# Performance work log

Hardware: AMD Instinct MI355X
Metric: run time of the kernel (lower is better)

The kernel has to match this reference:

```python
import jax, jax.numpy as jnp
from jax import lax
import numpy as np

B = 32768
H = 7
W = 7
EMB = 64
NUM_ACTIONS = 7
HIDDEN = 128
CNN_OUT = 64 * 3 * 3  # 576, from 7x7 input through the conv/pool stack


def setup_inputs() -> dict:
    key = jax.random.key(0)
    ks = jax.random.split(key, 20)
    frame = jax.random.randint(ks[0], (2, B, H, W, 3), 0, 11, dtype=jnp.int32)
    carried_col = jax.random.randint(ks[1], (2, B, 1), 0, 6, dtype=jnp.int32)
    carried_obj = jax.random.randint(ks[2], (2, B, 1), 0, 11, dtype=jnp.int32)

    def w(k, shape):
        return (jax.random.normal(k, shape, jnp.float32) * 0.05)

    return {
        "frame": frame,
        "carried_col": carried_col,
        "carried_obj": carried_obj,
        "conv1_w": w(ks[3], (16, 3, 2, 2)),  "conv1_b": jnp.zeros((16,), jnp.float32),
        "conv2_w": w(ks[4], (32, 16, 2, 2)), "conv2_b": jnp.zeros((32,), jnp.float32),
        "conv3_w": w(ks[5], (64, 32, 2, 2)), "conv3_b": jnp.zeros((64,), jnp.float32),
        "proj_w": w(ks[6], (EMB, CNN_OUT + 2)), "proj_b": jnp.zeros((EMB,), jnp.float32),
        "h1_w": w(ks[7], (HIDDEN, EMB * 2 + 4)), "h1_b": jnp.zeros((HIDDEN,), jnp.float32),
        "ln_g": jnp.ones((HIDDEN,), jnp.float32), "ln_b": jnp.zeros((HIDDEN,), jnp.float32),
        "h2_w": w(ks[8], (HIDDEN, HIDDEN)), "h2_b": jnp.zeros((HIDDEN,), jnp.float32),
        "h3_w": w(ks[9], (NUM_ACTIONS, HIDDEN)), "h3_b": jnp.zeros((NUM_ACTIONS,), jnp.float32),
    }


def _conv(x, wgt, b):
    # Conv2d(kernel=2, padding=1), NCHW
    y = lax.conv_general_dilated(x, wgt, (1, 1), [(1, 1), (1, 1)],
                                 dimension_numbers=("NCHW", "OIHW", "NCHW"))
    return y + b[None, :, None, None]


def _maxpool2(x):
    # MaxPool2d(2): window 2, stride 2, floor (VALID)
    return lax.reduce_window(x, -jnp.inf, lax.max, (1, 1, 2, 2), (1, 1, 2, 2), "VALID")


def _encode(fr, cc, co, p):
    x = fr.transpose(0, 3, 1, 2).astype(jnp.float32)  # [B,3,H,W]
    x = _maxpool2(jax.nn.relu(_conv(x, p["conv1_w"], p["conv1_b"])))  # [B,16,4,4]
    x = _maxpool2(jax.nn.relu(_conv(x, p["conv2_w"], p["conv2_b"])))  # [B,32,2,2]
    x = jax.nn.relu(_conv(x, p["conv3_w"], p["conv3_b"]))             # [B,64,3,3]
    feats = x.reshape(x.shape[0], -1)                                  # [B,576]
    carried = jnp.concatenate([cc, co], axis=-1).astype(jnp.float32)   # [B,2]
    comb = jnp.concatenate([feats, carried], axis=1)                   # [B,578]
    return jax.nn.relu(comb @ p["proj_w"].T + p["proj_b"])            # [B,64]


def _dir_pos(fr):
    # vectorized first-match of frame[...,0]==10 in row-major order
    b = fr.shape[0]
    mask = (fr[..., 0] == 10).reshape(b, -1)             # [B, H*W]
    has = jnp.any(mask, axis=-1)                         # [B]
    idx = jnp.argmax(mask, axis=-1)                      # first True (row-major)
    y = idx // W
    x = idx % W
    ch2 = fr[..., 2].reshape(b, -1)
    d_raw = jnp.take_along_axis(ch2, idx[:, None], axis=1)[:, 0] % 4
    d = jnp.where(has, d_raw, 0)                         # [B] int
    pos = jnp.stack([y.astype(jnp.float32) / (H - 1),
                     x.astype(jnp.float32) / (W - 1)], axis=-1)
    pos = jnp.where(has[:, None], pos, jnp.float32(0.5))  # [B,2]
    return d, pos


def _forward(frame, carried_col, carried_obj, p):
    curr_f, next_f = frame[0], frame[1]
    curr_emb = _encode(curr_f, carried_col[0], carried_obj[0], p)
    next_emb = _encode(next_f, carried_col[1], carried_obj[1], p)
    cd, cpos = _dir_pos(curr_f)
    nd, npos = _dir_pos(next_f)
    delta = ((nd - cd + 4) % 4).astype(jnp.float32)
    angle = delta * (2.0 * 3.14159 / 4.0)  # matches source constant
    dir_delta = jnp.stack([jnp.sin(angle), jnp.cos(angle)], axis=-1)  # [B,2]
    pos_delta = npos - cpos                                           # [B,2]
    comb = jnp.concatenate([curr_emb, next_emb, dir_delta, pos_delta], axis=-1)  # [B,132]
    h = comb @ p["h1_w"].T + p["h1_b"]
    mu = h.mean(-1, keepdims=True)
    var = ((h - mu) ** 2).mean(-1, keepdims=True)
    h = (h - mu) * lax.rsqrt(var + 1e-5) * p["ln_g"] + p["ln_b"]
    h = jax.nn.relu(h)  # dropout = identity in eval
    h = jax.nn.relu(h @ p["h2_w"].T + p["h2_b"])
    return h @ p["h3_w"].T + p["h3_b"]  # [B, num_actions]


def reference(frame, carried_col, carried_obj,
              conv1_w, conv1_b, conv2_w, conv2_b, conv3_w, conv3_b,
              proj_w, proj_b, h1_w, h1_b, ln_g, ln_b,
              h2_w, h2_b, h3_w, h3_b):
    p = dict(conv1_w=conv1_w, conv1_b=conv1_b, conv2_w=conv2_w, conv2_b=conv2_b,
             conv3_w=conv3_w, conv3_b=conv3_b, proj_w=proj_w, proj_b=proj_b,
             h1_w=h1_w, h1_b=h1_b, ln_g=ln_g, ln_b=ln_b,
             h2_w=h2_w, h2_b=h2_b, h3_w=h3_w, h3_b=h3_b)
    return _forward(frame, carried_col, carried_obj, p)
```

## Files before the change

### kernel.cpp

```cpp
#include <hip/hip_runtime.h>
#include <hip/hip_bf16.h>

#define BATCH 32768
#define NELEM 65536

typedef unsigned short u16;
typedef unsigned int u32;
typedef __attribute__((ext_vector_type(8))) short bf16x8;
typedef __attribute__((ext_vector_type(4))) float f32x4;

__device__ __forceinline__ float bf2f(u16 u) {
    union { u32 u; float f; } c; c.u = ((u32)u) << 16; return c.f;
}
__device__ __forceinline__ u16 f2bf(float f) {
    union { float f; u32 u; } c; c.f = f;
    u32 x = c.u;
    u32 r = (x + 0x7fffu + ((x >> 16) & 1u)) >> 16;
    return (u16)r;
}

__global__ __launch_bounds__(256) void k0_prep(const float* __restrict__ pw,
        const float* __restrict__ w2, const float* __restrict__ w3,
        const float* __restrict__ h2w, const float* __restrict__ h1w,
        const float* __restrict__ w1,
        u16* __restrict__ pwT, u16* __restrict__ w2r, u16* __restrict__ w3r,
        u16* __restrict__ h2hi, u16* __restrict__ h2lo,
        u16* __restrict__ h1hi, u16* __restrict__ h1lo,
        u16* __restrict__ w1hi, u16* __restrict__ w1lo) {
    int idx = blockIdx.x * 256 + threadIdx.x;
    if (idx < 38912) {
        int j = idx / 608, kk = idx - j * 608;
        float v = 0.f;
        if (kk < 576) {
            int p = kk >> 6, oc = kk & 63;
            v = pw[j * 578 + oc * 9 + p];
        } else if (kk < 578) {
            v = pw[j * 578 + kk];
        }
        pwT[idx] = f2bf(v);
    } else if (idx < 40960) {
        int i = idx - 38912;
        int oc = i >> 6, rem = i & 63, tap = rem >> 4, ic = rem & 15;
        w2r[i] = f2bf(w2[oc * 64 + ic * 4 + tap]);
    } else if (idx < 49152) {
        int i = idx - 40960;
        int oc = i >> 7, rem = i & 127, tap = rem >> 5, ic = rem & 31;
        w3r[i] = f2bf(w3[oc * 128 + ic * 4 + tap]);
    } else if (idx < 65536) {
        int i = idx - 49152;
        float v = h2w[i];
        u16 hi = f2bf(v);
        h2hi[i] = hi;
        h2lo[i] = f2bf(v - bf2f(hi));
    } else if (idx < 86016) {
        int i = idx - 65536;
        int j = i / 160, k = i - j * 160;
        float v = (k < 132) ? h1w[j * 132 + k] : 0.f;
        u16 hi = f2bf(v);
        h1hi[i] = hi;
        h1lo[i] = f2bf(v - bf2f(hi));
    } else if (idx < 86528) {
        int i = idx - 86016;
        int oc = i >> 5, k = i & 31;
        int ky = k >> 4, kx = (k >> 3) & 1, c = k & 7;
        float v = (c < 3) ? w1[oc * 12 + c * 4 + ky * 2 + kx] : 0.f;
        u16 hi = f2bf(v);
        w1hi[i] = hi;
        w1lo[i] = f2bf(v - bf2f(hi));
    }
}

__global__ __launch_bounds__(256) void kconv_all(const int* __restrict__ frame,
        const u16* __restrict__ w1hi, const u16* __restrict__ w1lo,
        const float* __restrict__ b1,
        const u16* __restrict__ w2r, const float* __restrict__ b2,
        const u16* __restrict__ w3r, const float* __restrict__ b3,
        const int* __restrict__ ccol, const int* __restrict__ cobj,
        const u16* __restrict__ pwT, const float* __restrict__ pb,
        float* __restrict__ comb, float4* __restrict__ fdir) {
    __shared__ u16 lds[24576];
    u16* p2L   = lds;
    u16* p1L   = lds + 4096;
    u16* frL   = lds + 12288;
    u16* featL = lds + 4096;
    int t = threadIdx.x;
    int l = t & 63;
    int wv = t >> 6;
    int col = l & 15;
    int kg = l >> 4;
    int e0 = blockIdx.x * 32;

    #pragma unroll
    for (int i = 0; i < 6; ++i) {
        int o = i * 256 + t;
        if (o < 1312) *(uint4*)(frL + o * 8) = make_uint4(0u, 0u, 0u, 0u);
    }

    {
        bf16x8 c1hi = *(const bf16x8*)(w1hi + col * 32 + kg * 8);
        bf16x8 c1lo = *(const bf16x8*)(w1lo + col * 32 + kg * 8);
        float c1b = b1[col];
        int ky1 = kg >> 1, kx1 = kg & 1;
        bool wr1 = (kg < 2);
        for (int h = 0; h < 2; ++h) {
            __syncthreads();
            const int* fbase = frame + (size_t)(e0 + h * 16) * 147;
            #pragma unroll
            for (int i = 0; i < 10; ++i) {
                int idx = i * 256 + t;
                if (idx < 2352) {
                    int le = idx / 147, r = idx - le * 147;
                    int cell = r / 3, c = r - cell * 3;
                    int y = cell / 7, x = cell - y * 7;
                    frL[le * 656 + (y + 1) * 72 + (x + 1) * 8 + c] = f2bf((float)fbase[idx]);
                }
            }
            __syncthreads();
            #pragma unroll
            for (int q = 0; q < 4; ++q) {
                int le = wv * 4 + q;
                const u16* eb = frL + le * 656;
                u16* op = p1L + (h * 16 + le) * 256;
                #pragma unroll
                for (int mt = 0; mt < 4; ++mt) {
                    int posA = mt * 16 + col;
                    int oy = posA >> 3, ox = posA & 7;
                    bf16x8 a = *(const bf16x8*)(eb + (oy + ky1) * 72 + (ox + kx1) * 8);
                    f32x4 acc = {0.f, 0.f, 0.f, 0.f};
                    acc = __builtin_amdgcn_mfma_f32_16x16x32_bf16(a, c1hi, acc, 0, 0, 0);
                    acc = __builtin_amdgcn_mfma_f32_16x16x32_bf16(a, c1lo, acc, 0, 0, 0);
                    float x0 = fmaxf(acc[0] + c1b, 0.f);
                    float x1 = fmaxf(acc[1] + c1b, 0.f);
                    float x2 = fmaxf(acc[2] + c1b, 0.f);
                    float x3 = fmaxf(acc[3] + c1b, 0.f);
                    float y0 = fmaxf(x0, x1);
                    float y1 = fmaxf(x2, x3);
                    float m0 = fmaxf(y0, __shfl_xor(y0, 32, 64));
                    float m1 = fmaxf(y1, __shfl_xor(y1, 32, 64));
                    if (wr1) {
                        op[(mt * 4 + kg * 2 + 0) * 16 + col] = f2bf(m0);
                        op[(mt * 4 + kg * 2 + 1) * 16 + col] = f2bf(m1);
                    }
                }
            }
            {
                int le = wv * 4 + kg;
                const u16* eb = frL + le * 656;
                int best = 49;
                #pragma unroll
                for (int q2 = 0; q2 < 4; ++q2) {
                    int cell = col + q2 * 16;
                    if (cell < 49) {
                        int y = cell / 7, x = cell - y * 7;
                        u16 v = eb[(y + 1) * 72 + (x + 1) * 8];
                        if (v == (u16)0x4120 && cell < best) best = cell;
                    }
                }
                best = min(best, __shfl_xor(best, 1, 64));
                best = min(best, __shfl_xor(best, 2, 64));
                best = min(best, __shfl_xor(best, 4, 64));
                best = min(best, __shfl_xor(best, 8, 64));
                if (col == 0) {
                    float dd = 0.f, py = 0.5f, px = 0.5f;
                    if (best < 49) {
                        int y = best / 7, x = best - y * 7;
                        u16 c2 = eb[(y + 1) * 72 + (x + 1) * 8 + 2];
                        dd = (float)(((int)bf2f(c2)) & 3);
                        py = (float)y / 6.0f;
                        px = (float)x / 6.0f;
                    }
                    fdir[e0 + h * 16 + le] = make_float4(dd, py, px, 0.f);
                }
            }
        }
    }
    __syncthreads();

    {
        bf16x8 bfrag[2][2];
        #pragma unroll
        for (int s = 0; s < 2; ++s)
            #pragma unroll
            for (int nt = 0; nt < 2; ++nt)
                bfrag[s][nt] = *(const bf16x8*)(w2r + (nt * 16 + col) * 64 + s * 32 + kg * 8);
        float bias2[2] = { b2[col], b2[16 + col] };
        int oy = col >> 2, ox = col & 3;
        int aoff[2]; bool aok[2];
        #pragma unroll
        for (int s = 0; s < 2; ++s) {
            int tap = 2 * s + (kg >> 1);
            int ky = tap >> 1, kx = tap & 1;
            int iy = oy - 1 + ky, ix = ox - 1 + kx;
            aok[s] = (iy >= 0 && ix >= 0);
            aoff[s] = (iy * 4 + ix) * 16 + (kg & 1) * 8;
        }
        #pragma unroll
        for (int q = 0; q < 8; ++q) {
            int e = wv * 8 + q;
            const u16* pbase = p1L + e * 256;
            bf16x8 a0 = {0,0,0,0,0,0,0,0}, a1 = {0,0,0,0,0,0,0,0};
            if (aok[0]) a0 = *(const bf16x8*)(pbase + aoff[0]);
            if (aok[1]) a1 = *(const bf16x8*)(pbase + aoff[1]);
            f32x4 acc0 = {0.f,0.f,0.f,0.f}, acc1 = {0.f,0.f,0.f,0.f};
            acc0 = __builtin_amdgcn_mfma_f32_16x16x32_bf16(a0, bfrag[0][0], acc0, 0, 0, 0);
            acc1 = __builtin_amdgcn_mfma_f32_16x16x32_bf16(a0, bfrag[0][1], acc1, 0, 0, 0);
            acc0 = __builtin_amdgcn_mfma_f32_16x16x32_bf16(a1, bfrag[1][0], acc0, 0, 0, 0);
            acc1 = __builtin_amdgcn_mfma_f32_16x16x32_bf16(a1, bfrag[1][1], acc1, 0, 0, 0);
            #pragma unroll
            for (int nt = 0; nt < 2; ++nt) {
                f32x4 acc = nt ? acc1 : acc0;
                float b = bias2[nt];
                float m0 = fmaxf(fmaxf(acc[0] + b, 0.f), fmaxf(acc[1] + b, 0.f));
                float m1 = fmaxf(fmaxf(acc[2] + b, 0.f), fmaxf(acc[3] + b, 0.f));
                float p0 = fmaxf(m0, __shfl_xor(m0, 16, 64));
                float p1 = fmaxf(m1, __shfl_xor(m1, 16, 64));
                if ((kg & 1) == 0) {
                    int qq = (kg >> 1) * 2;
                    u16* op = p2L + e * 128 + nt * 16 + col;
                    op[qq * 32]       = f2bf(p0);
                    op[(qq + 1) * 32] = f2bf(p1);
                }
            }
        }
    }
    __syncthreads();

    int colhi = col >> 3, collo = col & 7;
    {
        bf16x8 bfrag[4][4];
        #pragma unroll
        for (int s = 0; s < 4; ++s)
            #pragma unroll
            for (int nt = 0; nt < 4; ++nt)
                bfrag[s][nt] = *(const bf16x8*)(w3r + (nt * 16 + col) * 128 + s * 32 + kg * 8);
        float bias[4];
        #pragma unroll
        for (int nt = 0; nt < 4; ++nt) bias[nt] = b3[nt * 16 + col];

        auto do_tile = [&](int i) {
            int m0 = i * 16;
            int m = m0 + col;
            u32 elem = (u32)(((unsigned long long)(u32)m * 954437177ull) >> 33);
            int p = m - (int)elem * 9;
            int oy = (p * 86) >> 8;
            int ox = p - 3 * oy;
            const u16* pbase = p2L + elem * 128 + kg * 8;
            f32x4 acc[4];
            #pragma unroll
            for (int nt = 0; nt < 4; ++nt) {
                acc[nt][0] = 0.f; acc[nt][1] = 0.f; acc[nt][2] = 0.f; acc[nt][3] = 0.f;
            }
            #pragma unroll
            for (int s = 0; s < 4; ++s) {
                int ky = s >> 1, kx = s & 1;
                int iy = oy - 1 + ky, ix = ox - 1 + kx;
                bf16x8 a = {0,0,0,0,0,0,0,0};
                if (iy >= 0 && iy <= 1 && ix >= 0 && ix <= 1)
                    a = *(const bf16x8*)(pbase + (iy * 2 + ix) * 32);
                #pragma unroll
                for (int nt = 0; nt < 4; ++nt)
                    acc[nt] = __builtin_amdgcn_mfma_f32_16x16x32_bf16(a, bfrag[s][nt], acc[nt], 0, 0, 0);
            }
            #pragma unroll
            for (int r = 0; r < 4; ++r) {
                int mr = m0 + kg * 4 + r;
                u32 er = (u32)(((unsigned long long)(u32)mr * 954437177ull) >> 33);
                int pr = mr - (int)er * 9;
                int e7 = (int)(er & 7u);
                u16* fb = featL + er * 640 + collo;
                #pragma unroll
                for (int nt = 0; nt < 4; ++nt) {
                    int blk = (pr * 8 + nt * 2 + colhi) ^ e7;
                    fb[blk * 8] = f2bf(fmaxf(acc[nt][r] + bias[nt], 0.f));
                }
            }
        };
        #pragma unroll
        for (int u = 0; u < 4; ++u) do_tile(wv + u * 4);
        if (wv < 2) do_tile(16 + wv);
    }
    if (t < 32) {
        union { u16 s[8]; uint4 q; } b;
        b.s[0] = f2bf((float)ccol[e0 + t]);
        b.s[1] = f2bf((float)cobj[e0 + t]);
        #pragma unroll
        for (int i = 2; i < 8; ++i) b.s[i] = 0;
        *(uint4*)(featL + t * 640 + (72 ^ (t & 7)) * 8) = b.q;
    }
    __syncthreads();

    int rh = wv & 1, nh = wv >> 1;
    int m0g = e0 + rh * 16;
    const u16* arowb = featL + (rh * 16 + col) * 640;
    int rx = col & 7;
    const u16* brow = pwT + (nh * 32 + col) * 608 + kg * 8;
    f32x4 acc0 = {0.f,0.f,0.f,0.f}, acc1 = {0.f,0.f,0.f,0.f};
    #pragma unroll
    for (int k0 = 0; k0 < 608; k0 += 32) {
        bf16x8 a;
        if (k0 + kg * 8 < 584) {
            int L = (k0 >> 3) + kg;
            a = *(const bf16x8*)(arowb + (L ^ rx) * 8);
        } else {
            #pragma unroll
            for (int j = 0; j < 8; ++j) a[j] = 0;
        }
        bf16x8 b0 = *(const bf16x8*)(brow + k0);
        bf16x8 b1 = *(const bf16x8*)(brow + 16 * 608 + k0);
        acc0 = __builtin_amdgcn_mfma_f32_16x16x32_bf16(a, b0, acc0, 0, 0, 0);
        acc1 = __builtin_amdgcn_mfma_f32_16x16x32_bf16(a, b1, acc1, 0, 0, 0);
    }
    float* outbase = (m0g < BATCH) ? (comb + (size_t)m0g * 128)
                                   : (comb + (size_t)(m0g - BATCH) * 128 + 64);
    #pragma unroll
    for (int nt = 0; nt < 2; ++nt) {
        int n = nh * 32 + nt * 16 + col;
        float pbv = pb[n];
        f32x4 acc = nt ? acc1 : acc0;
        #pragma unroll
        for (int r = 0; r < 4; ++r) {
            outbase[(kg * 4 + r) * 128 + n] = fmaxf(acc[r] + pbv, 0.f);
        }
    }
}

__device__ __forceinline__ void split8(const float* __restrict__ x,
                                       bf16x8& hi, bf16x8& lo) {
    #pragma unroll
    for (int j = 0; j < 8; ++j) {
        u16 h = f2bf(x[j]);
        hi[j] = (short)h;
        lo[j] = (short)f2bf(x[j] - bf2f(h));
    }
}

__global__ __launch_bounds__(256) void kmlp(const float* __restrict__ comb,
        const float4* __restrict__ fdir,
        const u16* __restrict__ h1hi, const u16* __restrict__ h1lo,
        const float* __restrict__ h1b,
        const float* __restrict__ lng, const float* __restrict__ lnb,
        const u16* __restrict__ h2hi, const u16* __restrict__ h2lo,
        const float* __restrict__ h2b,
        const float* __restrict__ h3w, const float* __restrict__ h3b,
        float* __restrict__ out) {
    __shared__ float hL[64 * 132];
    int t = threadIdx.x;
    int l = t & 63;
    int col = l & 15;
    int kg = l >> 4;
    int wv = t >> 6;
    int mb = blockIdx.x * 64;

    {
        int gb = mb + wv * 16 + col;
        const float* arow = comb + (size_t)gb * 128 + kg * 8;
        const u16* bh = h1hi + col * 160 + kg * 8;
        const u16* bl = h1lo + col * 160 + kg * 8;
        f32x4 acc[8];
        #pragma unroll
        for (int nt = 0; nt < 8; ++nt) {
            acc[nt][0] = 0.f; acc[nt][1] = 0.f; acc[nt][2] = 0.f; acc[nt][3] = 0.f;
        }
        #pragma unroll
        for (int s = 0; s < 5; ++s) {
            float x[8];
            if (s < 4) {
                #pragma unroll
                for (int j = 0; j < 8; ++j) x[j] = arow[s * 32 + j];
            } else {
                #pragma unroll
                for (int j = 0; j < 8; ++j) x[j] = 0.f;
                if (kg == 0) {
                    float4 f0 = fdir[gb];
                    float4 f1 = fdir[gb + BATCH];
                    int delta = (((int)f1.x) - ((int)f0.x) + 4) & 3;
                    const float ANG = (float)(2.0 * 3.14159 / 4.0);
                    float angle = (float)delta * ANG;
                    x[0] = sinf(angle);
                    x[1] = cosf(angle);
                    x[2] = f1.y - f0.y;
                    x[3] = f1.z - f0.z;
                }
            }
            bf16x8 ahi, alo;
            split8(x, ahi, alo);
            #pragma unroll
            for (int nt = 0; nt < 8; ++nt) {
                bf16x8 bhiF = *(const bf16x8*)(bh + nt * 2560 + s * 32);
                bf16x8 bloF = *(const bf16x8*)(bl + nt * 2560 + s * 32);
                acc[nt] = __builtin_amdgcn_mfma_f32_16x16x32_bf16(ahi, bhiF, acc[nt], 0, 0, 0);
                acc[nt] = __builtin_amdgcn_mfma_f32_16x16x32_bf16(alo, bhiF, acc[nt], 0, 0, 0);
                acc[nt] = __builtin_amdgcn_mfma_f32_16x16x32_bf16(ahi, bloF, acc[nt], 0, 0, 0);
            }
        }
        #pragma unroll
        for (int nt = 0; nt < 8; ++nt) {
            float bv = h1b[nt * 16 + col];
            #pragma unroll
            for (int r = 0; r < 4; ++r)
                hL[(wv * 16 + kg * 4 + r) * 132 + nt * 16 + col] = acc[nt][r] + bv;
        }
    }
    __syncthreads();

    for (int rr = 0; rr < 16; ++rr) {
        float* rp = hL + (wv * 16 + rr) * 132 + l * 2;
        float2 v = *(const float2*)rp;
        float s = v.x + v.y;
        s += __shfl_xor(s, 1, 64);
        s += __shfl_xor(s, 2, 64);
        s += __shfl_xor(s, 4, 64);
        s += __shfl_xor(s, 8, 64);
        s += __shfl_xor(s, 16, 64);
        s += __shfl_xor(s, 32, 64);
        float mu = s * (1.0f / 128.0f);
        float d0 = v.x - mu, d1 = v.y - mu;
        float vs = d0 * d0 + d1 * d1;
        vs += __shfl_xor(vs, 1, 64);
        vs += __shfl_xor(vs, 2, 64);
        vs += __shfl_xor(vs, 4, 64);
        vs += __shfl_xor(vs, 8, 64);
        vs += __shfl_xor(vs, 16, 64);
        vs += __shfl_xor(vs, 32, 64);
        float rs = rsqrtf(vs * (1.0f / 128.0f) + 1e-5f);
        float2 o;
        o.x = fmaxf(d0 * rs * lng[l * 2]     + lnb[l * 2],     0.f);
        o.y = fmaxf(d1 * rs * lng[l * 2 + 1] + lnb[l * 2 + 1], 0.f);
        *(float2*)rp = o;
    }
    __syncthreads();

    {
        const float* arow = hL + (wv * 16 + col) * 132 + kg * 8;
        const u16* bh = h2hi + col * 128 + kg * 8;
        const u16* bl = h2lo + col * 128 + kg * 8;
        f32x4 acc[8];
        #pragma unroll
        for (int nt = 0; nt < 8; ++nt) {
            acc[nt][0] = 0.f; acc[nt][1] = 0.f; acc[nt][2] = 0.f; acc[nt][3] = 0.f;
        }
        #pragma unroll
        for (int s = 0; s < 4; ++s) {
            float x[8];
            #pragma unroll
            for (int j = 0; j < 8; ++j) x[j] = arow[s * 32 + j];
            bf16x8 ahi, alo;
            split8(x, ahi, alo);
            #pragma unroll
            for (int nt = 0; nt < 8; ++nt) {
                bf16x8 bhiF = *(const bf16x8*)(bh + nt * 2048 + s * 32);
                bf16x8 bloF = *(const bf16x8*)(bl + nt * 2048 + s * 32);
                acc[nt] = __builtin_amdgcn_mfma_f32_16x16x32_bf16(ahi, bhiF, acc[nt], 0, 0, 0);
                acc[nt] = __builtin_amdgcn_mfma_f32_16x16x32_bf16(alo, bhiF, acc[nt], 0, 0, 0);
                acc[nt] = __builtin_amdgcn_mfma_f32_16x16x32_bf16(ahi, bloF, acc[nt], 0, 0, 0);
            }
        }
        __syncthreads();
        #pragma unroll
        for (int nt = 0; nt < 8; ++nt) {
            float bv = h2b[nt * 16 + col];
            #pragma unroll
            for (int r = 0; r < 4; ++r)
                hL[(wv * 16 + kg * 4 + r) * 132 + nt * 16 + col] = fmaxf(acc[nt][r] + bv, 0.f);
        }
    }
    __syncthreads();

    {
        int row = t >> 2, jq = t & 3, j0 = jq * 2;
        const float* rp = hL + row * 132;
        float a0 = h3b[j0];
        float a1 = (jq < 3) ? h3b[j0 + 1] : 0.f;
        #pragma unroll 4
        for (int c = 0; c < 32; ++c) {
            float4 v = *(const float4*)(rp + c * 4);
            const float* wr0 = h3w + j0 * 128 + c * 4;
            a0 += v.x * wr0[0];
            a0 += v.y * wr0[1];
            a0 += v.z * wr0[2];
            a0 += v.w * wr0[3];
            if (jq < 3) {
                const float* wr1 = h3w + (j0 + 1) * 128 + c * 4;
                a1 += v.x * wr1[0];
                a1 += v.y * wr1[1];
                a1 += v.z * wr1[2];
                a1 += v.w * wr1[3];
            }
        }
        float* ob = out + (size_t)(mb + row) * 7;
        ob[j0] = a0;
        if (jq < 3) ob[j0 + 1] = a1;
    }
}

extern "C" void kernel_launch(void* const* d_in, const int* in_sizes, int n_in,
                              void* d_out, int out_size, void* d_ws, size_t ws_size,
                              hipStream_t stream) {
    const int*   frame = (const int*)d_in[0];
    const int*   ccol  = (const int*)d_in[1];
    const int*   cobj  = (const int*)d_in[2];
    const float* w1    = (const float*)d_in[3];
    const float* b1    = (const float*)d_in[4];
    const float* w2    = (const float*)d_in[5];
    const float* b2    = (const float*)d_in[6];
    const float* w3    = (const float*)d_in[7];
    const float* b3    = (const float*)d_in[8];
    const float* pw    = (const float*)d_in[9];
    const float* pb    = (const float*)d_in[10];
    const float* h1w   = (const float*)d_in[11];
    const float* h1b   = (const float*)d_in[12];
    const float* lng   = (const float*)d_in[13];
    const float* lnb   = (const float*)d_in[14];
    const float* h2w   = (const float*)d_in[15];
    const float* h2b   = (const float*)d_in[16];
    const float* h3w   = (const float*)d_in[17];
    const float* h3b   = (const float*)d_in[18];
    float* out = (float*)d_out;

    char* ws = (char*)d_ws;
    float* comb     = (float*)(ws + 0);
    float4* fdir    = (float4*)(ws + 33554432);
    u16*   pwT      = (u16*)(ws + 132120576);
    u16*   w2r      = (u16*)(ws + 132120576 + 131072);
    u16*   w3r      = (u16*)(ws + 132120576 + 139264);
    u16*   h2hi     = (u16*)(ws + 132120576 + 163840);
    u16*   h2lo     = (u16*)(ws + 132120576 + 196608);
    u16*   h1hi     = (u16*)(ws + 132120576 + 229376);
    u16*   h1lo     = (u16*)(ws + 132120576 + 270336);
    u16*   w1hi     = (u16*)(ws + 132120576 + 311296);
    u16*   w1lo     = (u16*)(ws + 132120576 + 312320);

    k0_prep<<<340, 256, 0, stream>>>(pw, w2, w3, h2w, h1w, w1,
                                     pwT, w2r, w3r, h2hi, h2lo, h1hi, h1lo,
                                     w1hi, w1lo);
    kconv_all<<<2048, 256, 0, stream>>>(frame, w1hi, w1lo, b1, w2r, b2,
                                        w3r, b3, ccol, cobj, pwT, pb, comb, fdir);
    kmlp<<<512, 256, 0, stream>>>(comb, fdir, h1hi, h1lo, h1b, lng, lnb,
                                  h2hi, h2lo, h2b, h3w, h3b, out);
}
```

Baseline: 231.0 us.

## Fuse conv encoder and MLP head into a single kernel via LDS handoff

Merges the conv/projection kernel and the MLP kernel into one. Each block now processes 16 batch items for both frames, so the current and next embeddings for a row sit in the same block. The comb and fdir intermediates stay in shared memory instead of going through global workspace, which removes a 16MB write and read plus one launch. In exchange the MLP stage works on only 16 rows per block, so each weight fetch is reused less and there are more barriers per block.

```diff
diff --git a/kernel.cpp b/kernel.cpp
--- a/kernel.cpp
+++ b/kernel.cpp
@@ -70,25 +70,44 @@
     }
 }
 
-__global__ __launch_bounds__(256) void kconv_all(const int* __restrict__ frame,
+__device__ __forceinline__ void split8(const float* __restrict__ x,
+                                       bf16x8& hi, bf16x8& lo) {
+    #pragma unroll
+    for (int j = 0; j < 8; ++j) {
+        u16 h = f2bf(x[j]);
+        hi[j] = (short)h;
+        lo[j] = (short)f2bf(x[j] - bf2f(h));
+    }
+}
+
+__global__ __launch_bounds__(256) void kall(const int* __restrict__ frame,
         const u16* __restrict__ w1hi, const u16* __restrict__ w1lo,
         const float* __restrict__ b1,
         const u16* __restrict__ w2r, const float* __restrict__ b2,
         const u16* __restrict__ w3r, const float* __restrict__ b3,
         const int* __restrict__ ccol, const int* __restrict__ cobj,
         const u16* __restrict__ pwT, const float* __restrict__ pb,
-        float* __restrict__ comb, float4* __restrict__ fdir) {
+        const u16* __restrict__ h1hi, const u16* __restrict__ h1lo,
+        const float* __restrict__ h1b,
+        const float* __restrict__ lng, const float* __restrict__ lnb,
+        const u16* __restrict__ h2hi, const u16* __restrict__ h2lo,
+        const float* __restrict__ h2b,
+        const float* __restrict__ h3w, const float* __restrict__ h3b,
+        float* __restrict__ out) {
     __shared__ u16 lds[24576];
+    __shared__ float4 fdirL[32];
     u16* p2L   = lds;
     u16* p1L   = lds + 4096;
     u16* frL   = lds + 12288;
     u16* featL = lds + 4096;
+    float* combL = (float*)lds;
+    float* hL    = (float*)(lds + 4096);
     int t = threadIdx.x;
     int l = t & 63;
     int wv = t >> 6;
     int col = l & 15;
     int kg = l >> 4;
-    int e0 = blockIdx.x * 32;
+    int b0 = blockIdx.x * 16;
 
     #pragma unroll
     for (int i = 0; i < 6; ++i) {
@@ -104,7 +123,7 @@
         bool wr1 = (kg < 2);
         for (int h = 0; h < 2; ++h) {
             __syncthreads();
-            const int* fbase = frame + (size_t)(e0 + h * 16) * 147;
+            const int* fbase = frame + ((size_t)b0 + (size_t)h * BATCH) * 147;
             #pragma unroll
             for (int i = 0; i < 10; ++i) {
                 int idx = i * 256 + t;
@@ -169,7 +188,7 @@
                         py = (float)y / 6.0f;
                         px = (float)x / 6.0f;
                     }
-                    fdir[e0 + h * 16 + le] = make_float4(dd, py, px, 0.f);
+                    fdirL[h * 16 + le] = make_float4(dd, py, px, 0.f);
                 }
             }
         }
@@ -280,87 +299,56 @@
         if (wv < 2) do_tile(16 + wv);
     }
     if (t < 32) {
+        int g = b0 + (t >> 4) * BATCH + (t & 15);
         union { u16 s[8]; uint4 q; } b;
-        b.s[0] = f2bf((float)ccol[e0 + t]);
-        b.s[1] = f2bf((float)cobj[e0 + t]);
+        b.s[0] = f2bf((float)ccol[g]);
+        b.s[1] = f2bf((float)cobj[g]);
         #pragma unroll
         for (int i = 2; i < 8; ++i) b.s[i] = 0;
         *(uint4*)(featL + t * 640 + (72 ^ (t & 7)) * 8) = b.q;
     }
     __syncthreads();
 
-    int rh = wv & 1, nh = wv >> 1;
-    int m0g = e0 + rh * 16;
-    const u16* arowb = featL + (rh * 16 + col) * 640;
-    int rx = col & 7;
-    const u16* brow = pwT + (nh * 32 + col) * 608 + kg * 8;
-    f32x4 acc0 = {0.f,0.f,0.f,0.f}, acc1 = {0.f,0.f,0.f,0.f};
-    #pragma unroll
-    for (int k0 = 0; k0 < 608; k0 += 32) {
-        bf16x8 a;
-        if (k0 + kg * 8 < 584) {
-            int L = (k0 >> 3) + kg;
-            a = *(const bf16x8*)(arowb + (L ^ rx) * 8);
-        } else {
-            #pragma unroll
-            for (int j = 0; j < 8; ++j) a[j] = 0;
-        }
-        bf16x8 b0 = *(const bf16x8*)(brow + k0);
-        bf16x8 b1 = *(const bf16x8*)(brow + 16 * 608 + k0);
-        acc0 = __builtin_amdgcn_mfma_f32_16x16x32_bf16(a, b0, acc0, 0, 0, 0);
-        acc1 = __builtin_amdgcn_mfma_f32_16x16x32_bf16(a, b1, acc1, 0, 0, 0);
-    }
-    float* outbase = (m0g < BATCH) ? (comb + (size_t)m0g * 128)
-                                   : (comb + (size_t)(m0g - BATCH) * 128 + 64);
-    #pragma unroll
-    for (int nt = 0; nt < 2; ++nt) {
-        int n = nh * 32 + nt * 16 + col;
-        float pbv = pb[n];
-        f32x4 acc = nt ? acc1 : acc0;
-        #pragma unroll
-        for (int r = 0; r < 4; ++r) {
-            outbase[(kg * 4 + r) * 128 + n] = fmaxf(acc[r] + pbv, 0.f);
-        }
-    }
-}
-
-__device__ __forceinline__ void split8(const float* __restrict__ x,
-                                       bf16x8& hi, bf16x8& lo) {
-    #pragma unroll
-    for (int j = 0; j < 8; ++j) {
-        u16 h = f2bf(x[j]);
-        hi[j] = (short)h;
-        lo[j] = (short)f2bf(x[j] - bf2f(h));
-    }
-}
-
-__global__ __launch_bounds__(256) void kmlp(const float* __restrict__ comb,
-        const float4* __restrict__ fdir,
-        const u16* __restrict__ h1hi, const u16* __restrict__ h1lo,
-        const float* __restrict__ h1b,
-        const float* __restrict__ lng, const float* __restrict__ lnb,
-        const u16* __restrict__ h2hi, const u16* __restrict__ h2lo,
-        const float* __restrict__ h2b,
-        const float* __restrict__ h3w, const float* __restrict__ h3b,
-        float* __restrict__ out) {
-    __shared__ float hL[64 * 132];
-    int t = threadIdx.x;
-    int l = t & 63;
-    int col = l & 15;
-    int kg = l >> 4;
-    int wv = t >> 6;
-    int mb = blockIdx.x * 64;
-
     {
-        int gb = mb + wv * 16 + col;
-        const float* arow = comb + (size_t)gb * 128 + kg * 8;
-        const u16* bh = h1hi + col * 160 + kg * 8;
-        const u16* bl = h1lo + col * 160 + kg * 8;
-        f32x4 acc[8];
-        #pragma unroll
-        for (int nt = 0; nt < 8; ++nt) {
-            acc[nt][0] = 0.f; acc[nt][1] = 0.f; acc[nt][2] = 0.f; acc[nt][3] = 0.f;
-        }
+        int rh = wv & 1, nh = wv >> 1;
+        const u16* arowb = featL + (rh * 16 + col) * 640;
+        int rx = col & 7;
+        const u16* brow = pwT + (nh * 32 + col) * 608 + kg * 8;
+        f32x4 acc0 = {0.f,0.f,0.f,0.f}, acc1 = {0.f,0.f,0.f,0.f};
+        #pragma unroll
+        for (int k0 = 0; k0 < 608; k0 += 32) {
+            bf16x8 a;
+            if (k0 + kg * 8 < 584) {
+                int L = (k0 >> 3) + kg;
+                a = *(const bf16x8*)(arowb + (L ^ rx) * 8);
+            } else {
+                #pragma unroll
+                for (int j = 0; j < 8; ++j) a[j] = 0;
+            }
+            bf16x8 b0f = *(const bf16x8*)(brow + k0);
+            bf16x8 b1f = *(const bf16x8*)(brow + 16 * 608 + k0);
+            acc0 = __builtin_amdgcn_mfma_f32_16x16x32_bf16(a, b0f, acc0, 0, 0, 0);
+            acc1 = __builtin_amdgcn_mfma_f32_16x16x32_bf16(a, b1f, acc1, 0, 0, 0);
+        }
+        __syncthreads();
+        #pragma unroll
+        for (int nt = 0; nt < 2; ++nt) {
+            int n = nh * 32 + nt * 16 + col;
+            float pbv = pb[n];
+            f32x4 acc = nt ? acc1 : acc0;
+            #pragma unroll
+            for (int r = 0; r < 4; ++r) {
+                combL[(kg * 4 + r) * 128 + rh * 64 + n] = fmaxf(acc[r] + pbv, 0.f);
+            }
+        }
+    }
+    __syncthreads();
+
+    {
+        const float* arow = combL + col * 128 + kg * 8;
+        f32x4 acc[2];
+        acc[0][0]=0.f; acc[0][1]=0.f; acc[0][2]=0.f; acc[0][3]=0.f;
+        acc[1][0]=0.f; acc[1][1]=0.f; acc[1][2]=0.f; acc[1][3]=0.f;
         #pragma unroll
         for (int s = 0; s < 5; ++s) {
             float x[8];
@@ -371,8 +359,8 @@
                 #pragma unroll
                 for (int j = 0; j < 8; ++j) x[j] = 0.f;
                 if (kg == 0) {
-                    float4 f0 = fdir[gb];
-                    float4 f1 = fdir[gb + BATCH];
+                    float4 f0 = fdirL[col];
+                    float4 f1 = fdirL[16 + col];
                     int delta = (((int)f1.x) - ((int)f0.x) + 4) & 3;
                     const float ANG = (float)(2.0 * 3.14159 / 4.0);
                     float angle = (float)delta * ANG;
@@ -385,26 +373,29 @@
             bf16x8 ahi, alo;
             split8(x, ahi, alo);
             #pragma unroll
-            for (int nt = 0; nt < 8; ++nt) {
-                bf16x8 bhiF = *(const bf16x8*)(bh + nt * 2560 + s * 32);
-                bf16x8 bloF = *(const bf16x8*)(bl + nt * 2560 + s * 32);
+            for (int nt = 0; nt < 2; ++nt) {
+                int n0 = (wv * 2 + nt) * 16 + col;
+                bf16x8 bhiF = *(const bf16x8*)(h1hi + n0 * 160 + s * 32 + kg * 8);
+                bf16x8 bloF = *(const bf16x8*)(h1lo + n0 * 160 + s * 32 + kg * 8);
                 acc[nt] = __builtin_amdgcn_mfma_f32_16x16x32_bf16(ahi, bhiF, acc[nt], 0, 0, 0);
                 acc[nt] = __builtin_amdgcn_mfma_f32_16x16x32_bf16(alo, bhiF, acc[nt], 0, 0, 0);
                 acc[nt] = __builtin_amdgcn_mfma_f32_16x16x32_bf16(ahi, bloF, acc[nt], 0, 0, 0);
             }
         }
         #pragma unroll
-        for (int nt = 0; nt < 8; ++nt) {
-            float bv = h1b[nt * 16 + col];
+        for (int nt = 0; nt < 2; ++nt) {
+            int n = (wv * 2 + nt) * 16 + col;
+            float bv = h1b[n];
             #pragma unroll
             for (int r = 0; r < 4; ++r)
-                hL[(wv * 16 + kg * 4 + r) * 132 + nt * 16 + col] = acc[nt][r] + bv;
-        }
-    }
-    __syncthreads();
-
-    for (int rr = 0; rr < 16; ++rr) {
-        float* rp = hL + (wv * 16 + rr) * 132 + l * 2;
+                hL[(kg * 4 + r) * 132 + n] = acc[nt][r] + bv;
+        }
+    }
+    __syncthreads();
+
+    #pragma unroll
+    for (int rr = 0; rr < 4; ++rr) {
+        float* rp = hL + (wv * 4 + rr) * 132 + l * 2;
         float2 v = *(const float2*)rp;
         float s = v.x + v.y;
         s += __shfl_xor(s, 1, 64);
@@ -431,14 +422,10 @@
     __syncthreads();
 
     {
-        const float* arow = hL + (wv * 16 + col) * 132 + kg * 8;
-        const u16* bh = h2hi + col * 128 + kg * 8;
-        const u16* bl = h2lo + col * 128 + kg * 8;
-        f32x4 acc[8];
-        #pragma unroll
-        for (int nt = 0; nt < 8; ++nt) {
-            acc[nt][0] = 0.f; acc[nt][1] = 0.f; acc[nt][2] = 0.f; acc[nt][3] = 0.f;
-        }
+        const float* arow = hL + col * 132 + kg * 8;
+        f32x4 acc[2];
+        acc[0][0]=0.f; acc[0][1]=0.f; acc[0][2]=0.f; acc[0][3]=0.f;
+        acc[1][0]=0.f; acc[1][1]=0.f; acc[1][2]=0.f; acc[1][3]=0.f;
         #pragma unroll
         for (int s = 0; s < 4; ++s) {
             float x[8];
@@ -447,9 +434,10 @@
             bf16x8 ahi, alo;
             split8(x, ahi, alo);
             #pragma unroll
-            for (int nt = 0; nt < 8; ++nt) {
-                bf16x8 bhiF = *(const bf16x8*)(bh + nt * 2048 + s * 32);
-                bf16x8 bloF = *(const bf16x8*)(bl + nt * 2048 + s * 32);
+            for (int nt = 0; nt < 2; ++nt) {
+                int n0 = (wv * 2 + nt) * 16 + col;
+                bf16x8 bhiF = *(const bf16x8*)(h2hi + n0 * 128 + s * 32 + kg * 8);
+                bf16x8 bloF = *(const bf16x8*)(h2lo + n0 * 128 + s * 32 + kg * 8);
                 acc[nt] = __builtin_amdgcn_mfma_f32_16x16x32_bf16(ahi, bhiF, acc[nt], 0, 0, 0);
                 acc[nt] = __builtin_amdgcn_mfma_f32_16x16x32_bf16(alo, bhiF, acc[nt], 0, 0, 0);
                 acc[nt] = __builtin_amdgcn_mfma_f32_16x16x32_bf16(ahi, bloF, acc[nt], 0, 0, 0);
@@ -457,39 +445,30 @@
         }
         __syncthreads();
         #pragma unroll
-        for (int nt = 0; nt < 8; ++nt) {
-            float bv = h2b[nt * 16 + col];
+        for (int nt = 0; nt < 2; ++nt) {
+            int n = (wv * 2 + nt) * 16 + col;
+            float bv = h2b[n];
             #pragma unroll
             for (int r = 0; r < 4; ++r)
-                hL[(wv * 16 + kg * 4 + r) * 132 + nt * 16 + col] = fmaxf(acc[nt][r] + bv, 0.f);
-        }
-    }
-    __syncthreads();
-
-    {
-        int row = t >> 2, jq = t & 3, j0 = jq * 2;
+                hL[(kg * 4 + r) * 132 + n] = fmaxf(acc[nt][r] + bv, 0.f);
+        }
+    }
+    __syncthreads();
+
+    if (t < 112) {
+        int row = t / 7, j = t - row * 7;
         const float* rp = hL + row * 132;
-        float a0 = h3b[j0];
-        float a1 = (jq < 3) ? h3b[j0 + 1] : 0.f;
+        float a0 = h3b[j];
+        const float* wr0 = h3w + j * 128;
         #pragma unroll 4
         for (int c = 0; c < 32; ++c) {
             float4 v = *(const float4*)(rp + c * 4);
-            const float* wr0 = h3w + j0 * 128 + c * 4;
-            a0 += v.x * wr0[0];
-            a0 += v.y * wr0[1];
-            a0 += v.z * wr0[2];
-            a0 += v.w * wr0[3];
-            if (jq < 3) {
-                const float* wr1 = h3w + (j0 + 1) * 128 + c * 4;
-                a1 += v.x * wr1[0];
-                a1 += v.y * wr1[1];
-                a1 += v.z * wr1[2];
-                a1 += v.w * wr1[3];
-            }
-        }
-        float* ob = out + (size_t)(mb + row) * 7;
-        ob[j0] = a0;
-        if (jq < 3) ob[j0 + 1] = a1;
+            a0 += v.x * wr0[c * 4 + 0];
+            a0 += v.y * wr0[c * 4 + 1];
+            a0 += v.z * wr0[c * 4 + 2];
+            a0 += v.w * wr0[c * 4 + 3];
+        }
+        out[(size_t)(b0 + row) * 7 + j] = a0;
     }
 }
 
@@ -518,23 +497,21 @@
     float* out = (float*)d_out;
 
     char* ws = (char*)d_ws;
-    float* comb     = (float*)(ws + 0);
-    float4* fdir    = (float4*)(ws + 33554432);
-    u16*   pwT      = (u16*)(ws + 132120576);
-    u16*   w2r      = (u16*)(ws + 132120576 + 131072);
-    u16*   w3r      = (u16*)(ws + 132120576 + 139264);
-    u16*   h2hi     = (u16*)(ws + 132120576 + 163840);
-    u16*   h2lo     = (u16*)(ws + 132120576 + 196608);
-    u16*   h1hi     = (u16*)(ws + 132120576 + 229376);
-    u16*   h1lo     = (u16*)(ws + 132120576 + 270336);
-    u16*   w1hi     = (u16*)(ws + 132120576 + 311296);
-    u16*   w1lo     = (u16*)(ws + 132120576 + 312320);
+    u16*   pwT      = (u16*)(ws + 0);
+    u16*   w2r      = (u16*)(ws + 131072);
+    u16*   w3r      = (u16*)(ws + 139264);
+    u16*   h2hi     = (u16*)(ws + 163840);
+    u16*   h2lo     = (u16*)(ws + 196608);
+    u16*   h1hi     = (u16*)(ws + 229376);
+    u16*   h1lo     = (u16*)(ws + 270336);
+    u16*   w1hi     = (u16*)(ws + 311296);
+    u16*   w1lo     = (u16*)(ws + 312320);
 
     k0_prep<<<340, 256, 0, stream>>>(pw, w2, w3, h2w, h1w, w1,
                                      pwT, w2r, w3r, h2hi, h2lo, h1hi, h1lo,
                                      w1hi, w1lo);
-    kconv_all<<<2048, 256, 0, stream>>>(frame, w1hi, w1lo, b1, w2r, b2,
-                                        w3r, b3, ccol, cobj, pwT, pb, comb, fdir);
-    kmlp<<<512, 256, 0, stream>>>(comb, fdir, h1hi, h1lo, h1b, lng, lnb,
-                                  h2hi, h2lo, h2b, h3w, h3b, out);
+    kall<<<2048, 256, 0, stream>>>(frame, w1hi, w1lo, b1, w2r, b2,
+                                   w3r, b3, ccol, cobj, pwT, pb,
+                                   h1hi, h1lo, h1b, lng, lnb,
+                                   h2hi, h2lo, h2b, h3w, h3b, out);
 }
```

After: 219.3 us (median of 2 runs). -5.1%, faster.
